# Performance work log

Measured on AMD Instinct MI355X. Metric: run time of the kernel, lower is better.

Reference implementation:

```python
import math
import jax, jax.numpy as jnp
import numpy as np

D_MODEL = 1024
N_HEADS = 16
HEAD_DIM = D_MODEL // N_HEADS  # 64
QDIM = HEAD_DIM // 4           # 16
SPIKE_SLOPE = 5.0
B, S = 2, 2048


def _qweight(r, i, j, k):
    # Hamilton-product weight matrix, identical to QLinear.forward's torch.cat construction.
    return jnp.concatenate([
        jnp.concatenate([r, -i, -j, -k], 1),
        jnp.concatenate([i, r, -k, j], 1),
        jnp.concatenate([j, k, r, -i], 1),
        jnp.concatenate([k, -j, i, r], 1),
    ], 0)


def setup_inputs() -> dict:
    key = jax.random.key(0)
    ks = jax.random.split(key, 20)
    Qo = Qi = D_MODEL // 4  # 256
    p = lambda k, shape, s=0.02: (jax.random.normal(k, shape, dtype=jnp.float32) * s)
    inp = {
        'query': jax.random.normal(ks[0], (B, S, D_MODEL), dtype=jnp.float32),
        'key_in': jax.random.normal(ks[1], (B, S, D_MODEL), dtype=jnp.float32),
        'value': jax.random.normal(ks[2], (B, S, D_MODEL), dtype=jnp.float32),
        'mask': jnp.ones((B, S), dtype=jnp.int32),
        'density_feat': jax.random.normal(ks[3], (B, S, 3), dtype=jnp.float32),
        # q_proj QLinear params
        'wq_r': p(ks[4], (Qo, Qi)), 'wq_i': p(ks[5], (Qo, Qi)),
        'wq_j': p(ks[6], (Qo, Qi)), 'wq_k': p(ks[7], (Qo, Qi)),
        'bq': jnp.zeros((D_MODEL,), jnp.float32),
        # k_proj QLinear params
        'wk_r': p(ks[8], (Qo, Qi)), 'wk_i': p(ks[9], (Qo, Qi)),
        'wk_j': p(ks[10], (Qo, Qi)), 'wk_k': p(ks[11], (Qo, Qi)),
        'bk': jnp.zeros((D_MODEL,), jnp.float32),
        # v_proj / out_proj dense params
        'wv': p(ks[12], (D_MODEL, D_MODEL)), 'bv': jnp.zeros((D_MODEL,), jnp.float32),
        'wo': p(ks[13], (D_MODEL, D_MODEL)), 'bo': jnp.zeros((D_MODEL,), jnp.float32),
        # learned spike threshold (init -1.0 as in torch)
        'threshold': jnp.asarray(-1.0, dtype=jnp.float32),
        # density_mod MLP (use nonzero values so the gate shift is exercised)
        'dm1_w': p(ks[14], (16, 3), 0.5), 'dm1_b': p(ks[15], (16,), 0.1),
        'dm2_w': p(ks[16], (1, 16), 0.5), 'dm2_b': p(ks[17], (1,), 0.1),
    }
    return inp


def reference(query, key_in, value, mask, density_feat,
              wq_r, wq_i, wq_j, wq_k, bq,
              wk_r, wk_i, wk_j, wk_k, bk,
              wv, bv, wo, bo, threshold,
              dm1_w, dm1_b, dm2_w, dm2_b):
    H, hd, Qd = N_HEADS, HEAD_DIM, QDIM
    Bq, Sq, D = query.shape

    Wq = _qweight(wq_r, wq_i, wq_j, wq_k)
    Wk = _qweight(wk_r, wk_i, wk_j, wk_k)
    q = query @ Wq.T + bq
    k = key_in @ Wk.T + bk
    v = value @ wv.T + bv

    # head-major split, matching torch.cat(x.split(hd, -1), dim=0)
    qh = q.reshape(Bq, Sq, H, hd).transpose(2, 0, 1, 3)  # (H,B,S,hd)
    kh = k.reshape(Bq, Sq, H, hd).transpose(2, 0, 1, 3)
    vh = v.reshape(Bq, Sq, H, hd).transpose(2, 0, 1, 3)

    # sum of 4 quaternion-component dot products == full dot product over hd
    scores = jnp.einsum('hbmd,hbnd->hbmn', qh, kh) / math.sqrt(Qd)
    scores = jnp.clip(scores, -6.0, 6.0)

    base_threshold = jax.nn.softplus(threshold)
    h1 = jax.nn.gelu(density_feat @ dm1_w.T + dm1_b, approximate=False)
    d_shift = (h1 @ dm2_w.T + dm2_b)[..., 0]  # (B,N)
    thr = base_threshold + d_shift[None, :, None, :] * 0.1  # (1,B,1,N)

    spike_gate = jax.nn.sigmoid(SPIKE_SLOPE * (scores - thr))
    mod = scores * (1.0 + spike_gate * 2.0)

    m2 = (mask[:, :, None] * mask[:, None, :])[None]  # (1,B,N,N)
    mod = jnp.where(m2 == 0, -10000.0, mod)

    weights = jax.nn.softmax(jnp.clip(mod, -30.0, 30.0), axis=-1)
    # dropout: eval mode (identity)
    out_h = jnp.einsum('hbmn,hbnd->hbmd', weights, vh)
    out = out_h.transpose(1, 2, 0, 3).reshape(Bq, Sq, D)
    return out @ wo.T + bo
```

## Files before the change

### kernel.cpp

```cpp
#include <hip/hip_runtime.h>
#include <stdint.h>
#include <math.h>

#define BB 2
#define SS 2048
#define DM 1024
#define NH 16
#define HD 64
#define MTOT (BB*SS)

typedef __bf16 bf16x8 __attribute__((ext_vector_type(8)));
typedef float  f32x4  __attribute__((ext_vector_type(4)));
typedef float  f32x2  __attribute__((ext_vector_type(2)));
typedef uint32_t u32x4 __attribute__((ext_vector_type(4)));

__device__ __forceinline__ unsigned short f2bf(float f) {
  __bf16 h = (__bf16)f;
  return __builtin_bit_cast(unsigned short, h);
}

__device__ __forceinline__ bf16x8 ldsv8(const unsigned short* p) {
  return __builtin_bit_cast(bf16x8, *(const u32x4*)p);
}

__device__ __forceinline__ void gl16(const void* g, void* l) {
  __builtin_amdgcn_global_load_lds(
      (const __attribute__((address_space(1))) uint32_t*)g,
      (__attribute__((address_space(3))) uint32_t*)l, 16, 0, 0);
}

#define MFMA16(a,b,c) __builtin_amdgcn_mfma_f32_16x16x32_bf16((a),(b),(c),0,0,0)

#define C_NEG5L2E  (-7.213475204444817f)
#define C_L2E      (1.4426950408889634f)
#define C_18L2E    (25.968510736001341f)

__device__ __forceinline__ f32x2 gate_pk(f32x2 s2, float kth, f32x2& lr) {
  s2 = __builtin_elementwise_min(__builtin_elementwise_max(s2, (f32x2){-6.f,-6.f}), (f32x2){6.f,6.f});
  const f32x2 targ = __builtin_elementwise_fma(s2, (f32x2){C_NEG5L2E, C_NEG5L2E}, (f32x2){kth, kth});
  f32x2 t;
  t.x = __builtin_amdgcn_exp2f(targ.x);
  t.y = __builtin_amdgcn_exp2f(targ.y);
  const f32x2 den = t + (f32x2){1.f, 1.f};
  f32x2 g;
  g.x = __builtin_amdgcn_rcpf(den.x);
  g.y = __builtin_amdgcn_rcpf(den.y);
  const f32x2 md = __builtin_elementwise_fma(s2 + s2, g, s2);
  const f32x2 pa = __builtin_elementwise_fma(md, (f32x2){C_L2E, C_L2E}, (f32x2){-C_18L2E, -C_18L2E});
  f32x2 p;
  p.x = __builtin_amdgcn_exp2f(pa.x);
  p.y = __builtin_amdgcn_exp2f(pa.y);
  lr += p;
  return p;
}

__global__ __launch_bounds__(256) void prep_all(
    const float* __restrict__ wqr, const float* __restrict__ wqi,
    const float* __restrict__ wqj, const float* __restrict__ wqk,
    const float* __restrict__ wkr, const float* __restrict__ wki,
    const float* __restrict__ wkj, const float* __restrict__ wkk,
    const float* __restrict__ wv,  const float* __restrict__ wo,
    unsigned short* __restrict__ Wq, unsigned short* __restrict__ Wk,
    unsigned short* __restrict__ Wv, unsigned short* __restrict__ Wo,
    const float* __restrict__ query, const float* __restrict__ key_in,
    const float* __restrict__ value,
    unsigned short* __restrict__ qcv, unsigned short* __restrict__ kcv,
    unsigned short* __restrict__ vcv,
    const float* __restrict__ density, const float* __restrict__ dm1w,
    const float* __restrict__ dm1b, const float* __restrict__ dm2w,
    const float* __restrict__ dm2b, const float* __restrict__ thr_s,
    const int* __restrict__ mask, float2* __restrict__ klim,
    int* __restrict__ amask)
{
  const int bid = blockIdx.x;
  if (bid < 512) {
    const int idx = (bid * 256 + threadIdx.x) * 8;
    const int o = idx >> 10, i = idx & 1023;
    const int br = o >> 8, bc = i >> 8;
    const int ro = o & 255, ci = i & 255;
    const int comp[4][4] = {{0,1,2,3},{1,0,3,2},{2,3,0,1},{3,2,1,0}};
    const float sgn[4][4] = {{1.f,-1.f,-1.f,-1.f},{1.f,1.f,-1.f,1.f},{1.f,1.f,1.f,-1.f},{1.f,-1.f,1.f,1.f}};
    const float* pq[4] = {wqr, wqi, wqj, wqk};
    const float* pk[4] = {wkr, wki, wkj, wkk};
    const int c_ = comp[br][bc];
    const float s_ = sgn[br][bc];
    const float* qsrc = pq[c_] + ro * 256 + ci;
    const float* ksrc = pk[c_] + ro * 256 + ci;
    {
      const float4 f0 = *(const float4*)qsrc;
      const float4 f1 = *(const float4*)(qsrc + 4);
      union { unsigned short us[8]; u32x4 v; } t;
      t.us[0]=f2bf(s_*f0.x); t.us[1]=f2bf(s_*f0.y); t.us[2]=f2bf(s_*f0.z); t.us[3]=f2bf(s_*f0.w);
      t.us[4]=f2bf(s_*f1.x); t.us[5]=f2bf(s_*f1.y); t.us[6]=f2bf(s_*f1.z); t.us[7]=f2bf(s_*f1.w);
      *(u32x4*)(Wq + idx) = t.v;
    }
    {
      const float4 f0 = *(const float4*)ksrc;
      const float4 f1 = *(const float4*)(ksrc + 4);
      union { unsigned short us[8]; u32x4 v; } t;
      t.us[0]=f2bf(s_*f0.x); t.us[1]=f2bf(s_*f0.y); t.us[2]=f2bf(s_*f0.z); t.us[3]=f2bf(s_*f0.w);
      t.us[4]=f2bf(s_*f1.x); t.us[5]=f2bf(s_*f1.y); t.us[6]=f2bf(s_*f1.z); t.us[7]=f2bf(s_*f1.w);
      *(u32x4*)(Wk + idx) = t.v;
    }
    {
      const float4 f0 = *(const float4*)(wv + idx);
      const float4 f1 = *(const float4*)(wv + idx + 4);
      union { unsigned short us[8]; u32x4 v; } t;
      t.us[0]=f2bf(f0.x); t.us[1]=f2bf(f0.y); t.us[2]=f2bf(f0.z); t.us[3]=f2bf(f0.w);
      t.us[4]=f2bf(f1.x); t.us[5]=f2bf(f1.y); t.us[6]=f2bf(f1.z); t.us[7]=f2bf(f1.w);
      *(u32x4*)(Wv + idx) = t.v;
    }
    {
      const float4 f0 = *(const float4*)(wo + idx);
      const float4 f1 = *(const float4*)(wo + idx + 4);
      union { unsigned short us[8]; u32x4 v; } t;
      t.us[0]=f2bf(f0.x); t.us[1]=f2bf(f0.y); t.us[2]=f2bf(f0.z); t.us[3]=f2bf(f0.w);
      t.us[4]=f2bf(f1.x); t.us[5]=f2bf(f1.y); t.us[6]=f2bf(f1.z); t.us[7]=f2bf(f1.w);
      *(u32x4*)(Wo + idx) = t.v;
    }
  } else if (bid < 2560) {
    const int i8 = ((bid - 512) * 256 + threadIdx.x) * 8;
    {
      const float4 f0 = *(const float4*)(query + i8);
      const float4 f1 = *(const float4*)(query + i8 + 4);
      union { unsigned short us[8]; u32x4 v; } t;
      t.us[0]=f2bf(f0.x); t.us[1]=f2bf(f0.y); t.us[2]=f2bf(f0.z); t.us[3]=f2bf(f0.w);
      t.us[4]=f2bf(f1.x); t.us[5]=f2bf(f1.y); t.us[6]=f2bf(f1.z); t.us[7]=f2bf(f1.w);
      *(u32x4*)(qcv + i8) = t.v;
    }
    {
      const float4 f0 = *(const float4*)(key_in + i8);
      const float4 f1 = *(const float4*)(key_in + i8 + 4);
      union { unsigned short us[8]; u32x4 v; } t;
      t.us[0]=f2bf(f0.x); t.us[1]=f2bf(f0.y); t.us[2]=f2bf(f0.z); t.us[3]=f2bf(f0.w);
      t.us[4]=f2bf(f1.x); t.us[5]=f2bf(f1.y); t.us[6]=f2bf(f1.z); t.us[7]=f2bf(f1.w);
      *(u32x4*)(kcv + i8) = t.v;
    }
    {
      const float4 f0 = *(const float4*)(value + i8);
      const float4 f1 = *(const float4*)(value + i8 + 4);
      union { unsigned short us[8]; u32x4 v; } t;
      t.us[0]=f2bf(f0.x); t.us[1]=f2bf(f0.y); t.us[2]=f2bf(f0.z); t.us[3]=f2bf(f0.w);
      t.us[4]=f2bf(f1.x); t.us[5]=f2bf(f1.y); t.us[6]=f2bf(f1.z); t.us[7]=f2bf(f1.w);
      *(u32x4*)(vcv + i8) = t.v;
    }
  } else {
    const int i = (bid - 2560) * 256 + threadIdx.x;
    if (i >= BB * SS) return;
    const float x0 = density[i*3+0], x1 = density[i*3+1], x2 = density[i*3+2];
    const float base = log1pf(expf(thr_s[0]));
    float acc = dm2b[0];
    #pragma unroll
    for (int j = 0; j < 16; ++j) {
      const float hj = dm1w[j*3+0]*x0 + dm1w[j*3+1]*x1 + dm1w[j*3+2]*x2 + dm1b[j];
      const float ge = 0.5f * hj * (1.0f + erff(hj * 0.70710678118654752f));
      acc += dm2w[j] * ge;
    }
    const float thr = base + 0.1f * acc;
    const int mk = mask[i];
    klim[i] = make_float2(thr * (-C_NEG5L2E),
                          mk ? 1e30f : -30.0f);
    const unsigned long long any = __ballot(mk == 0);
    if ((threadIdx.x & 63) == 0 && any)
      atomicOr(&amask[i >> 11], 1);
  }
}

struct GemmArgs {
  const unsigned short* A[3];
  const unsigned short* W[3];
  const float* bias[3];
  void* out[3];
  float scale[3];
  int omode[3];
};

template<int DB>
__global__ __launch_bounds__(256) void gemm_bt(GemmArgs args)
{
  __shared__ __align__(16) unsigned short lA[DB + 1][128*64];
  __shared__ __align__(16) unsigned short lB[DB + 1][128*64];
  const int z = blockIdx.y;
  const int tid = threadIdx.x;
  const int wid = tid >> 6, lane = tid & 63;
  const int l15 = lane & 15, l4 = lane >> 4;
  const int bm = blockIdx.x & 31, bn = blockIdx.x >> 5;
  const int row0 = bm * 128, col0 = bn * 128;
  const int wm = (wid >> 1) * 64, wn = (wid & 1) * 64;

  const unsigned short* gA[4];
  const unsigned short* gB[4];
  #pragma unroll
  for (int i = 0; i < 4; ++i) {
    const int c = (wid * 4 + i) * 64 + lane;
    const int r = c >> 3, jx = c & 7, j = jx ^ (r & 7);
    gA[i] = args.A[z] + (row0 + r) * 1024 + j * 8;
    gB[i] = args.W[z] + (col0 + r) * 1024 + j * 8;
  }

  f32x4 acc[4][4];
  #pragma unroll
  for (int i = 0; i < 4; ++i)
    #pragma unroll
    for (int j = 0; j < 4; ++j) acc[i][j] = (f32x4){0.f,0.f,0.f,0.f};

  #pragma unroll
  for (int i = 0; i < 4; ++i) {
    gl16(gA[i], &lA[0][(wid * 4 + i) * 512]);
    gl16(gB[i], &lB[0][(wid * 4 + i) * 512]);
  }
  if (DB) __syncthreads();

  for (int kt = 0; kt < 16; ++kt) {
    const int cb = DB ? (kt & 1) : 0;
    if (DB) {
      if (kt < 15) {
        const int nb = cb ^ 1, k0 = (kt + 1) * 64;
        #pragma unroll
        for (int i = 0; i < 4; ++i) {
          gl16(gA[i] + k0, &lA[nb][(wid * 4 + i) * 512]);
          gl16(gB[i] + k0, &lB[nb][(wid * 4 + i) * 512]);
        }
      }
    } else {
      if (kt > 0) {
        const int k0 = kt * 64;
        #pragma unroll
        for (int i = 0; i < 4; ++i) {
          gl16(gA[i] + k0, &lA[0][(wid * 4 + i) * 512]);
          gl16(gB[i] + k0, &lB[0][(wid * 4 + i) * 512]);
        }
      }
      __syncthreads();
    }
    #pragma unroll
    for (int kk = 0; kk < 2; ++kk) {
      const int kl = kk * 32 + l4 * 8;
      bf16x8 af[4], bfb[4];
      #pragma unroll
      for (int mi = 0; mi < 4; ++mi) {
        const int r = wm + mi * 16 + l15;
        af[mi] = ldsv8(&lA[cb][r * 64 + (kl ^ ((r & 7) << 3))]);
      }
      #pragma unroll
      for (int nj = 0; nj < 4; ++nj) {
        const int r = wn + nj * 16 + l15;
        bfb[nj] = ldsv8(&lB[cb][r * 64 + (kl ^ ((r & 7) << 3))]);
      }
      #pragma unroll
      for (int mi = 0; mi < 4; ++mi)
        #pragma unroll
        for (int nj = 0; nj < 4; ++nj)
          acc[mi][nj] = MFMA16(af[mi], bfb[nj], acc[mi][nj]);
    }
    __syncthreads();
  }

  const int om = args.omode[z];
  const float sc = args.scale[z];
  void* Cptr = args.out[z];
  #pragma unroll
  for (int nj = 0; nj < 4; ++nj) {
    const int c = col0 + wn + nj * 16 + l15;
    const float bv_ = args.bias[z][c];
    #pragma unroll
    for (int mi = 0; mi < 4; ++mi) {
      const int rb = row0 + wm + mi * 16 + l4 * 4;
      #pragma unroll
      for (int e = 0; e < 4; ++e) {
        const float val = (acc[mi][nj][e] + bv_) * sc;
        const int r = rb + e;
        if (om == 0) {
          ((unsigned short*)Cptr)[r * 1024 + c] = f2bf(val);
        } else if (om == 2) {
          ((float*)Cptr)[r * 1024 + c] = val;
        } else {
          const int h = c >> 6, d = c & 63, b = r >> 11, s = r & 2047;
          ((unsigned short*)Cptr)[((h * BB + b) * HD + d) * SS + s] = f2bf(val);
        }
      }
    }
  }
}

__global__ __launch_bounds__(512) void attn_kernel(
    const unsigned short* __restrict__ qg, const unsigned short* __restrict__ kg,
    const unsigned short* __restrict__ vT, const float2* __restrict__ klim,
    const int* __restrict__ mask, const int* __restrict__ amask,
    unsigned short* __restrict__ outg)
{
  __shared__ __align__(16) unsigned short smem[20480];
  unsigned char* sb = (unsigned char*)smem;
  unsigned short* lK = smem;
  unsigned short* lV = smem + 8192;
  unsigned short* lP = smem + 16384;

  const int tid = threadIdx.x;
  const int wid = tid >> 6, lane = tid & 63;
  const int l15 = lane & 15, l4 = lane >> 4;
  const int rg = wid >> 1, par = wid & 1;
  const int hb = blockIdx.x & 31, qb = blockIdx.x >> 5;
  const int h = hb >> 1, b = hb & 1;
  const int qr0 = qb * 64 + rg * 16;

  const unsigned short* kbase = kg + (b * SS) * DM + h * HD;
  const unsigned short* vbase = vT + ((h * BB + b) * HD) * SS;
  const float2* klimb = klim + b * SS;
  const int clean = (amask[b] == 0);

  const int kp   = wid >> 2;
  const int krho = ((wid & 3) << 3) | (lane >> 3);
  const int kj   = (lane & 7) ^ ((krho >> 1) & 7);
  const unsigned short* ksrc = kbase + (kp * 32 + krho) * DM + kj * 8;
  const int vq   = wid >> 2;
  const int vd   = ((wid & 3) << 4) | (lane >> 2);
  const int vc   = (lane & 3) ^ (vd & 3);
  const unsigned short* vsrc = vbase + (size_t)vd * SS + vq * 32 + vc * 8;
  unsigned char* kdw = sb + wid * 1024;
  unsigned char* vdw = sb + 16384 + wid * 1024;

  bf16x8 aq[2];
  {
    const unsigned short* qs = qg + (b * SS + qr0 + l15) * DM + h * HD + l4 * 8;
    aq[0] = __builtin_bit_cast(bf16x8, *(const u32x4*)qs);
    aq[1] = __builtin_bit_cast(bf16x8, *(const u32x4*)(qs + 32));
  }
  float limq[4];
  if (!clean) {
    #pragma unroll
    for (int e = 0; e < 4; ++e)
      limq[e] = mask[b * SS + qr0 + l4 * 4 + e] ? 1e30f : -30.0f;
  }

  f32x2 lr01 = {0.f, 0.f}, lr23 = {0.f, 0.f};
  f32x4 o[4];
  #pragma unroll
  for (int d = 0; d < 4; ++d) o[d] = (f32x4){0.f,0.f,0.f,0.f};

  unsigned short* lPw = lP + wid * 512;

  gl16(ksrc, kdw);
  gl16(vsrc, vdw);
  __syncthreads();

  #pragma unroll 2
  for (int pr = 0; pr < 32; ++pr) {
    const int cur = pr & 1;
    const unsigned short* lKt = lK + cur * 4096 + par * 2048;
    const unsigned short* lVt = lV + cur * 4096 + par * 2048;
    const int n0 = pr * 64 + par * 32;

    if (pr < 31) {
      const int nxt = cur ^ 1;
      gl16(ksrc + (size_t)(pr + 1) * 64 * DM, kdw + nxt * 8192);
      gl16(vsrc + (pr + 1) * 64,              vdw + nxt * 8192);
    }

    const float4 klA = *(const float4*)(klimb + n0 + 2 * l15);

    f32x4 sv[2];
    __builtin_amdgcn_s_setprio(1);
    #pragma unroll
    for (int cf = 0; cf < 2; ++cf) {
      f32x4 a = (f32x4){0.f,0.f,0.f,0.f};
      const int r = 2 * l15 + cf;
      #pragma unroll
      for (int kk = 0; kk < 2; ++kk)
        a = MFMA16(aq[kk], ldsv8(&lKt[r * 64 + ((kk * 32 + l4 * 8) ^ ((l15 & 7) << 3))]), a);
      sv[cf] = a;
    }
    __builtin_amdgcn_s_setprio(0);

    f32x2 p01[2], p23[2];
    if (clean) {
      #pragma unroll
      for (int cf = 0; cf < 2; ++cf) {
        const float kth = cf ? klA.z : klA.x;
        p01[cf] = gate_pk((f32x2){sv[cf][0], sv[cf][1]}, kth, lr01);
        p23[cf] = gate_pk((f32x2){sv[cf][2], sv[cf][3]}, kth, lr23);
      }
    } else {
      #pragma unroll
      for (int cf = 0; cf < 2; ++cf) {
        const float kth = cf ? klA.z : klA.x;
        const float klm = cf ? klA.w : klA.y;
        float pe[4];
        #pragma unroll
        for (int e = 0; e < 4; ++e) {
          float s = fminf(fmaxf(sv[cf][e], -6.f), 6.f);
          const float t = __builtin_amdgcn_exp2f(fmaf(s, C_NEG5L2E, kth));
          const float g = __builtin_amdgcn_rcpf(1.f + t);
          float md = fmaf(s + s, g, s);
          md = fminf(md, fminf(klm, limq[e]));
          pe[e] = __builtin_amdgcn_exp2f(fmaf(md, C_L2E, -C_18L2E));
        }
        p01[cf] = (f32x2){pe[0], pe[1]};
        p23[cf] = (f32x2){pe[2], pe[3]};
        lr01 += p01[cf];
        lr23 += p23[cf];
      }
    }

    #pragma unroll
    for (int e = 0; e < 4; ++e) {
      const int rr = l4 * 4 + e;
      const float pa_ = (e < 2) ? p01[0][e] : p23[0][e - 2];
      const float pb_ = (e < 2) ? p01[1][e] : p23[1][e - 2];
      union { unsigned short us[2]; unsigned int u; } pk2;
      pk2.us[0] = f2bf(pa_);
      pk2.us[1] = f2bf(pb_);
      *(unsigned int*)&lPw[rr * 32 + ((2 * l15) ^ ((rr & 3) << 3))] = pk2.u;
    }
    asm volatile("s_waitcnt lgkmcnt(0)" ::: "memory");
    __builtin_amdgcn_sched_barrier(0);

    const bf16x8 pa = ldsv8(&lPw[l15 * 32 + ((l4 * 8) ^ ((l15 & 3) << 3))]);

    __builtin_amdgcn_s_setprio(1);
    #pragma unroll
    for (int df = 0; df < 4; ++df) {
      const int d = df * 16 + l15;
      o[df] = MFMA16(pa, ldsv8(&lVt[d * 32 + ((l4 * 8) ^ ((d & 3) << 3))]), o[df]);
    }
    __builtin_amdgcn_s_setprio(0);

    __syncthreads();
  }

  float lrun[4] = {lr01.x, lr01.y, lr23.x, lr23.y};
  __syncthreads();
  float* xch = (float*)smem;
  float* slot = xch + rg * 1280;
  if (par) {
    #pragma unroll
    for (int df = 0; df < 4; ++df)
      *(f32x4*)&slot[(df * 64 + lane) * 4] = o[df];
    f32x4 lr;
    lr[0] = lrun[0]; lr[1] = lrun[1]; lr[2] = lrun[2]; lr[3] = lrun[3];
    *(f32x4*)&slot[1024 + lane * 4] = lr;
  }
  __syncthreads();
  if (!par) {
    #pragma unroll
    for (int df = 0; df < 4; ++df) {
      const f32x4 t = *(const f32x4*)&slot[(df * 64 + lane) * 4];
      o[df][0] += t[0]; o[df][1] += t[1]; o[df][2] += t[2]; o[df][3] += t[3];
    }
    const f32x4 lr = *(const f32x4*)&slot[1024 + lane * 4];
    #pragma unroll
    for (int e = 0; e < 4; ++e) {
      float ls = lrun[e] + lr[e];
      ls += __shfl_xor(ls, 1);
      ls += __shfl_xor(ls, 2);
      ls += __shfl_xor(ls, 4);
      ls += __shfl_xor(ls, 8);
      const float rl = __builtin_amdgcn_rcpf(ls);
      const int r = qr0 + l4 * 4 + e;
      #pragma unroll
      for (int df = 0; df < 4; ++df) {
        outg[(b * SS + r) * DM + h * HD + df * 16 + l15] = f2bf(o[df][e] * rl);
      }
    }
  }
}

extern "C" void kernel_launch(void* const* d_in, const int* in_sizes, int n_in,
                              void* d_out, int out_size, void* d_ws, size_t ws_size,
                              hipStream_t stream)
{
  const float* query   = (const float*)d_in[0];
  const float* key_in  = (const float*)d_in[1];
  const float* value   = (const float*)d_in[2];
  const int*   mask    = (const int*)d_in[3];
  const float* density = (const float*)d_in[4];
  const float* wq_r = (const float*)d_in[5];
  const float* wq_i = (const float*)d_in[6];
  const float* wq_j = (const float*)d_in[7];
  const float* wq_k = (const float*)d_in[8];
  const float* bq   = (const float*)d_in[9];
  const float* wk_r = (const float*)d_in[10];
  const float* wk_i = (const float*)d_in[11];
  const float* wk_j = (const float*)d_in[12];
  const float* wk_k = (const float*)d_in[13];
  const float* bk   = (const float*)d_in[14];
  const float* wv   = (const float*)d_in[15];
  const float* bv   = (const float*)d_in[16];
  const float* wo   = (const float*)d_in[17];
  const float* bo   = (const float*)d_in[18];
  const float* thrs = (const float*)d_in[19];
  const float* dm1w = (const float*)d_in[20];
  const float* dm1b = (const float*)d_in[21];
  const float* dm2w = (const float*)d_in[22];
  const float* dm2b = (const float*)d_in[23];

  char* ws = (char*)d_ws;
  unsigned short* Wq  = (unsigned short*)(ws + ((size_t)0 << 20));
  unsigned short* Wk  = (unsigned short*)(ws + ((size_t)2 << 20));
  unsigned short* Wv  = (unsigned short*)(ws + ((size_t)4 << 20));
  unsigned short* Wo  = (unsigned short*)(ws + ((size_t)6 << 20));
  unsigned short* qbf = (unsigned short*)(ws + ((size_t)8 << 20));
  unsigned short* kbf = (unsigned short*)(ws + ((size_t)16 << 20));
  unsigned short* vT  = (unsigned short*)(ws + ((size_t)24 << 20));
  unsigned short* att = (unsigned short*)(ws + ((size_t)32 << 20));
  float2* klim        = (float2*)(ws + ((size_t)40 << 20));
  int* amask          = (int*)(ws + ((size_t)40 << 20) + 65536);

  unsigned short* qcv = (unsigned short*)d_out;
  unsigned short* kcv = (unsigned short*)d_out + (size_t)MTOT * DM;
  unsigned short* vcv = att;

  hipMemsetAsync(amask, 0, 2 * sizeof(int), stream);
  prep_all<<<2576, 256, 0, stream>>>(
      wq_r, wq_i, wq_j, wq_k, wk_r, wk_i, wk_j, wk_k, wv, wo,
      Wq, Wk, Wv, Wo,
      query, key_in, value, qcv, kcv, vcv,
      density, dm1w, dm1b, dm2w, dm2b, thrs, mask, klim, amask);

  GemmArgs qkv;
  qkv.A[0] = qcv; qkv.W[0] = Wq; qkv.bias[0] = bq; qkv.out[0] = qbf; qkv.scale[0] = 0.25f; qkv.omode[0] = 0;
  qkv.A[1] = kcv; qkv.W[1] = Wk; qkv.bias[1] = bk; qkv.out[1] = kbf; qkv.scale[1] = 1.0f;  qkv.omode[1] = 0;
  qkv.A[2] = vcv; qkv.W[2] = Wv; qkv.bias[2] = bv; qkv.out[2] = vT;  qkv.scale[2] = 1.0f;  qkv.omode[2] = 1;
  gemm_bt<0><<<dim3(256, 3), 256, 0, stream>>>(qkv);

  attn_kernel<<<1024, 512, 0, stream>>>(qbf, kbf, vT, klim, mask, amask, att);

  GemmArgs og;
  og.A[0] = att; og.W[0] = Wo; og.bias[0] = bo; og.out[0] = d_out; og.scale[0] = 1.0f; og.omode[0] = 2;
  og.A[1] = att; og.W[1] = Wo; og.bias[1] = bo; og.out[1] = d_out; og.scale[1] = 1.0f; og.omode[1] = 2;
  og.A[2] = att; og.W[2] = Wo; og.bias[2] = bo; og.out[2] = d_out; og.scale[2] = 1.0f; og.omode[2] = 2;
  gemm_bt<1><<<dim3(256, 1), 256, 0, stream>>>(og);
}
```

Measured before the change: 180.5 us.

## Process two query sub-tiles per wave in attention, halving block threads

The attention kernel now runs 4 waves per block instead of 8, and each wave handles 32 query rows as two 16-row sub-tiles. Each wave reuses every K and V fragment read from LDS across both sub-tiles, and each thread issues two global-to-LDS copies per operand instead of one. The aim is to cut LDS read traffic per MFMA and raise arithmetic intensity per wave. The cost is more registers per wave (doubled accumulators and scores) and fewer waves per block to hide latency, with launch bounds set to 256 threads and 4 blocks per CU.

New measurement: 176.6 us, median of 2. 2.2% less time.

```diff
diff --git a/kernel.cpp b/kernel.cpp
--- a/kernel.cpp
+++ b/kernel.cpp
@@ -283,7 +283,7 @@
   }
 }
 
-__global__ __launch_bounds__(512) void attn_kernel(
+__global__ __launch_bounds__(256, 4) void attn_kernel(
     const unsigned short* __restrict__ qg, const unsigned short* __restrict__ kg,
     const unsigned short* __restrict__ vT, const float2* __restrict__ klim,
     const int* __restrict__ mask, const int* __restrict__ amask,
@@ -301,46 +301,55 @@
   const int rg = wid >> 1, par = wid & 1;
   const int hb = blockIdx.x & 31, qb = blockIdx.x >> 5;
   const int h = hb >> 1, b = hb & 1;
-  const int qr0 = qb * 64 + rg * 16;
+  const int qr0 = qb * 64 + rg * 32;
 
   const unsigned short* kbase = kg + (b * SS) * DM + h * HD;
   const unsigned short* vbase = vT + ((h * BB + b) * HD) * SS;
   const float2* klimb = klim + b * SS;
   const int clean = (amask[b] == 0);
 
-  const int kp   = wid >> 2;
-  const int krho = ((wid & 3) << 3) | (lane >> 3);
-  const int kj   = (lane & 7) ^ ((krho >> 1) & 7);
-  const unsigned short* ksrc = kbase + (kp * 32 + krho) * DM + kj * 8;
-  const int vq   = wid >> 2;
-  const int vd   = ((wid & 3) << 4) | (lane >> 2);
-  const int vc   = (lane & 3) ^ (vd & 3);
-  const unsigned short* vsrc = vbase + (size_t)vd * SS + vq * 32 + vc * 8;
-  unsigned char* kdw = sb + wid * 1024;
-  unsigned char* vdw = sb + 16384 + wid * 1024;
-
-  bf16x8 aq[2];
-  {
-    const unsigned short* qs = qg + (b * SS + qr0 + l15) * DM + h * HD + l4 * 8;
-    aq[0] = __builtin_bit_cast(bf16x8, *(const u32x4*)qs);
-    aq[1] = __builtin_bit_cast(bf16x8, *(const u32x4*)(qs + 32));
-  }
-  float limq[4];
+  const int krho = wid * 8 + (lane >> 3);
+  const int kc   = (lane & 7) ^ ((krho >> 1) & 7);
+  const unsigned short* ksrc0 = kbase + (size_t)krho * DM + kc * 8;
+  const unsigned short* ksrc1 = kbase + (size_t)(32 + krho) * DM + kc * 8;
+  const int vd_  = wid * 16 + (lane >> 2);
+  const int vc   = (lane & 3) ^ (vd_ & 3);
+  const unsigned short* vsrc0 = vbase + (size_t)vd_ * SS + vc * 8;
+  const unsigned short* vsrc1 = vbase + (size_t)vd_ * SS + 32 + vc * 8;
+  unsigned char* kd0 = sb + wid * 1024;
+  unsigned char* kd1 = sb + 4096 + wid * 1024;
+  unsigned char* vd0 = sb + 16384 + wid * 1024;
+  unsigned char* vd1 = sb + 16384 + 4096 + wid * 1024;
+
+  bf16x8 aq[2][2];
+  #pragma unroll
+  for (int sr = 0; sr < 2; ++sr) {
+    const unsigned short* qs = qg + (b * SS + qr0 + sr * 16 + l15) * DM + h * HD + l4 * 8;
+    aq[sr][0] = __builtin_bit_cast(bf16x8, *(const u32x4*)qs);
+    aq[sr][1] = __builtin_bit_cast(bf16x8, *(const u32x4*)(qs + 32));
+  }
+  float limq[2][4];
   if (!clean) {
     #pragma unroll
-    for (int e = 0; e < 4; ++e)
-      limq[e] = mask[b * SS + qr0 + l4 * 4 + e] ? 1e30f : -30.0f;
-  }
-
-  f32x2 lr01 = {0.f, 0.f}, lr23 = {0.f, 0.f};
-  f32x4 o[4];
+    for (int sr = 0; sr < 2; ++sr)
+      #pragma unroll
+      for (int e = 0; e < 4; ++e)
+        limq[sr][e] = mask[b * SS + qr0 + sr * 16 + l4 * 4 + e] ? 1e30f : -30.0f;
+  }
+
+  f32x2 lr01[2] = {{0.f,0.f},{0.f,0.f}}, lr23[2] = {{0.f,0.f},{0.f,0.f}};
+  f32x4 o[2][4];
   #pragma unroll
-  for (int d = 0; d < 4; ++d) o[d] = (f32x4){0.f,0.f,0.f,0.f};
-
-  unsigned short* lPw = lP + wid * 512;
-
-  gl16(ksrc, kdw);
-  gl16(vsrc, vdw);
+  for (int sr = 0; sr < 2; ++sr)
+    #pragma unroll
+    for (int d = 0; d < 4; ++d) o[sr][d] = (f32x4){0.f,0.f,0.f,0.f};
+
+  unsigned short* lPw = lP + wid * 1024;
+
+  gl16(ksrc0, kd0);
+  gl16(ksrc1, kd1);
+  gl16(vsrc0, vd0);
+  gl16(vsrc1, vd1);
   __syncthreads();
 
   #pragma unroll 2
@@ -351,114 +360,136 @@
     const int n0 = pr * 64 + par * 32;
 
     if (pr < 31) {
-      const int nxt = cur ^ 1;
-      gl16(ksrc + (size_t)(pr + 1) * 64 * DM, kdw + nxt * 8192);
-      gl16(vsrc + (pr + 1) * 64,              vdw + nxt * 8192);
+      const int co = (cur ^ 1) * 8192;
+      const size_t ko = (size_t)(pr + 1) * 64 * DM;
+      gl16(ksrc0 + ko, kd0 + co);
+      gl16(ksrc1 + ko, kd1 + co);
+      gl16(vsrc0 + (pr + 1) * 64, vd0 + co);
+      gl16(vsrc1 + (pr + 1) * 64, vd1 + co);
     }
 
     const float4 klA = *(const float4*)(klimb + n0 + 2 * l15);
 
-    f32x4 sv[2];
+    f32x4 sv[2][2];
     __builtin_amdgcn_s_setprio(1);
     #pragma unroll
     for (int cf = 0; cf < 2; ++cf) {
-      f32x4 a = (f32x4){0.f,0.f,0.f,0.f};
       const int r = 2 * l15 + cf;
-      #pragma unroll
-      for (int kk = 0; kk < 2; ++kk)
-        a = MFMA16(aq[kk], ldsv8(&lKt[r * 64 + ((kk * 32 + l4 * 8) ^ ((l15 & 7) << 3))]), a);
-      sv[cf] = a;
+      const bf16x8 kf0 = ldsv8(&lKt[r * 64 + ((l4 * 8) ^ ((l15 & 7) << 3))]);
+      const bf16x8 kf1 = ldsv8(&lKt[r * 64 + ((32 + l4 * 8) ^ ((l15 & 7) << 3))]);
+      #pragma unroll
+      for (int sr = 0; sr < 2; ++sr) {
+        f32x4 a = (f32x4){0.f,0.f,0.f,0.f};
+        a = MFMA16(aq[sr][0], kf0, a);
+        a = MFMA16(aq[sr][1], kf1, a);
+        sv[sr][cf] = a;
+      }
     }
     __builtin_amdgcn_s_setprio(0);
 
-    f32x2 p01[2], p23[2];
+    f32x2 p01[2][2], p23[2][2];
     if (clean) {
       #pragma unroll
-      for (int cf = 0; cf < 2; ++cf) {
-        const float kth = cf ? klA.z : klA.x;
-        p01[cf] = gate_pk((f32x2){sv[cf][0], sv[cf][1]}, kth, lr01);
-        p23[cf] = gate_pk((f32x2){sv[cf][2], sv[cf][3]}, kth, lr23);
-      }
+      for (int sr = 0; sr < 2; ++sr)
+        #pragma unroll
+        for (int cf = 0; cf < 2; ++cf) {
+          const float kth = cf ? klA.z : klA.x;
+          p01[sr][cf] = gate_pk((f32x2){sv[sr][cf][0], sv[sr][cf][1]}, kth, lr01[sr]);
+          p23[sr][cf] = gate_pk((f32x2){sv[sr][cf][2], sv[sr][cf][3]}, kth, lr23[sr]);
+        }
     } else {
       #pragma unroll
-      for (int cf = 0; cf < 2; ++cf) {
-        const float kth = cf ? klA.z : klA.x;
-        const float klm = cf ? klA.w : klA.y;
-        float pe[4];
+      for (int sr = 0; sr < 2; ++sr)
         #pragma unroll
-        for (int e = 0; e < 4; ++e) {
-          float s = fminf(fmaxf(sv[cf][e], -6.f), 6.f);
-          const float t = __builtin_amdgcn_exp2f(fmaf(s, C_NEG5L2E, kth));
-          const float g = __builtin_amdgcn_rcpf(1.f + t);
-          float md = fmaf(s + s, g, s);
-          md = fminf(md, fminf(klm, limq[e]));
-          pe[e] = __builtin_amdgcn_exp2f(fmaf(md, C_L2E, -C_18L2E));
+        for (int cf = 0; cf < 2; ++cf) {
+          const float kth = cf ? klA.z : klA.x;
+          const float klm = cf ? klA.w : klA.y;
+          float pe[4];
+          #pragma unroll
+          for (int e = 0; e < 4; ++e) {
+            float s = fminf(fmaxf(sv[sr][cf][e], -6.f), 6.f);
+            const float t = __builtin_amdgcn_exp2f(fmaf(s, C_NEG5L2E, kth));
+            const float g = __builtin_amdgcn_rcpf(1.f + t);
+            float md = fmaf(s + s, g, s);
+            md = fminf(md, fminf(klm, limq[sr][e]));
+            pe[e] = __builtin_amdgcn_exp2f(fmaf(md, C_L2E, -C_18L2E));
+          }
+          p01[sr][cf] = (f32x2){pe[0], pe[1]};
+          p23[sr][cf] = (f32x2){pe[2], pe[3]};
+          lr01[sr] += p01[sr][cf];
+          lr23[sr] += p23[sr][cf];
         }
-        p01[cf] = (f32x2){pe[0], pe[1]};
-        p23[cf] = (f32x2){pe[2], pe[3]};
-        lr01 += p01[cf];
-        lr23 += p23[cf];
-      }
-    }
-
-    #pragma unroll
-    for (int e = 0; e < 4; ++e) {
-      const int rr = l4 * 4 + e;
-      const float pa_ = (e < 2) ? p01[0][e] : p23[0][e - 2];
-      const float pb_ = (e < 2) ? p01[1][e] : p23[1][e - 2];
-      union { unsigned short us[2]; unsigned int u; } pk2;
-      pk2.us[0] = f2bf(pa_);
-      pk2.us[1] = f2bf(pb_);
-      *(unsigned int*)&lPw[rr * 32 + ((2 * l15) ^ ((rr & 3) << 3))] = pk2.u;
-    }
+    }
+
+    #pragma unroll
+    for (int sr = 0; sr < 2; ++sr)
+      #pragma unroll
+      for (int e = 0; e < 4; ++e) {
+        const int rr = l4 * 4 + e;
+        const float pa_ = (e < 2) ? p01[sr][0][e] : p23[sr][0][e - 2];
+        const float pb_ = (e < 2) ? p01[sr][1][e] : p23[sr][1][e - 2];
+        union { unsigned short us[2]; unsigned int u; } pk2;
+        pk2.us[0] = f2bf(pa_);
+        pk2.us[1] = f2bf(pb_);
+        *(unsigned int*)&lPw[sr * 512 + rr * 32 + ((2 * l15) ^ ((rr & 3) << 3))] = pk2.u;
+      }
     asm volatile("s_waitcnt lgkmcnt(0)" ::: "memory");
     __builtin_amdgcn_sched_barrier(0);
 
-    const bf16x8 pa = ldsv8(&lPw[l15 * 32 + ((l4 * 8) ^ ((l15 & 3) << 3))]);
+    const bf16x8 pa0 = ldsv8(&lPw[l15 * 32 + ((l4 * 8) ^ ((l15 & 3) << 3))]);
+    const bf16x8 pa1 = ldsv8(&lPw[512 + l15 * 32 + ((l4 * 8) ^ ((l15 & 3) << 3))]);
 
     __builtin_amdgcn_s_setprio(1);
     #pragma unroll
     for (int df = 0; df < 4; ++df) {
       const int d = df * 16 + l15;
-      o[df] = MFMA16(pa, ldsv8(&lVt[d * 32 + ((l4 * 8) ^ ((d & 3) << 3))]), o[df]);
+      const bf16x8 vf = ldsv8(&lVt[d * 32 + ((l4 * 8) ^ ((d & 3) << 3))]);
+      o[0][df] = MFMA16(pa0, vf, o[0][df]);
+      o[1][df] = MFMA16(pa1, vf, o[1][df]);
     }
     __builtin_amdgcn_s_setprio(0);
 
     __syncthreads();
   }
 
-  float lrun[4] = {lr01.x, lr01.y, lr23.x, lr23.y};
   __syncthreads();
   float* xch = (float*)smem;
-  float* slot = xch + rg * 1280;
+  float* slot = xch + rg * 2560;
   if (par) {
     #pragma unroll
-    for (int df = 0; df < 4; ++df)
-      *(f32x4*)&slot[(df * 64 + lane) * 4] = o[df];
-    f32x4 lr;
-    lr[0] = lrun[0]; lr[1] = lrun[1]; lr[2] = lrun[2]; lr[3] = lrun[3];
-    *(f32x4*)&slot[1024 + lane * 4] = lr;
+    for (int sr = 0; sr < 2; ++sr) {
+      #pragma unroll
+      for (int df = 0; df < 4; ++df)
+        *(f32x4*)&slot[((sr * 4 + df) * 64 + lane) * 4] = o[sr][df];
+      f32x4 lr;
+      lr[0] = lr01[sr].x; lr[1] = lr01[sr].y; lr[2] = lr23[sr].x; lr[3] = lr23[sr].y;
+      *(f32x4*)&slot[2048 + (sr * 64 + lane) * 4] = lr;
+    }
   }
   __syncthreads();
   if (!par) {
     #pragma unroll
-    for (int df = 0; df < 4; ++df) {
-      const f32x4 t = *(const f32x4*)&slot[(df * 64 + lane) * 4];
-      o[df][0] += t[0]; o[df][1] += t[1]; o[df][2] += t[2]; o[df][3] += t[3];
-    }
-    const f32x4 lr = *(const f32x4*)&slot[1024 + lane * 4];
-    #pragma unroll
-    for (int e = 0; e < 4; ++e) {
-      float ls = lrun[e] + lr[e];
-      ls += __shfl_xor(ls, 1);
-      ls += __shfl_xor(ls, 2);
-      ls += __shfl_xor(ls, 4);
-      ls += __shfl_xor(ls, 8);
-      const float rl = __builtin_amdgcn_rcpf(ls);
-      const int r = qr0 + l4 * 4 + e;
+    for (int sr = 0; sr < 2; ++sr) {
       #pragma unroll
       for (int df = 0; df < 4; ++df) {
-        outg[(b * SS + r) * DM + h * HD + df * 16 + l15] = f2bf(o[df][e] * rl);
+        const f32x4 t = *(const f32x4*)&slot[((sr * 4 + df) * 64 + lane) * 4];
+        o[sr][df][0] += t[0]; o[sr][df][1] += t[1]; o[sr][df][2] += t[2]; o[sr][df][3] += t[3];
+      }
+      const f32x4 lrq = *(const f32x4*)&slot[2048 + (sr * 64 + lane) * 4];
+      const float lrun[4] = {lr01[sr].x, lr01[sr].y, lr23[sr].x, lr23[sr].y};
+      #pragma unroll
+      for (int e = 0; e < 4; ++e) {
+        float ls = lrun[e] + lrq[e];
+        ls += __shfl_xor(ls, 1);
+        ls += __shfl_xor(ls, 2);
+        ls += __shfl_xor(ls, 4);
+        ls += __shfl_xor(ls, 8);
+        const float rl = __builtin_amdgcn_rcpf(ls);
+        const int r = qr0 + sr * 16 + l4 * 4 + e;
+        #pragma unroll
+        for (int df = 0; df < 4; ++df) {
+          outg[(b * SS + r) * DM + h * HD + df * 16 + l15] = f2bf(o[sr][df][e] * rl);
+        }
       }
     }
   }
@@ -522,7 +553,7 @@
   qkv.A[2] = vcv; qkv.W[2] = Wv; qkv.bias[2] = bv; qkv.out[2] = vT;  qkv.scale[2] = 1.0f;  qkv.omode[2] = 1;
   gemm_bt<0><<<dim3(256, 3), 256, 0, stream>>>(qkv);
 
-  attn_kernel<<<1024, 512, 0, stream>>>(qbf, kbf, vT, klim, mask, amask, att);
+  attn_kernel<<<1024, 256, 0, stream>>>(qbf, kbf, vT, klim, mask, amask, att);
 
   GemmArgs og;
   og.A[0] = att; og.W[0] = Wo; og.bias[0] = bo; og.out[0] = d_out; og.scale[0] = 1.0f; og.omode[0] = 2;
```
